# Kernel tuning notes

Hardware: AMD Instinct MI355X
Metric: run time of the kernel (lower is better)

## Reference

```python
import jax, jax.numpy as jnp
import numpy as np

L, B, S, E, H, V = 2, 64, 64, 1024, 1024, 32000


def _uni(key, shape, k):
    return jax.random.uniform(key, shape, jnp.float32, -k, k)


def setup_inputs() -> dict:
    key = jax.random.key(0)
    ks = jax.random.split(key, 16)
    k = 1.0 / np.sqrt(H)
    inp = {
        "inputs": jax.random.randint(ks[0], (S, B), 0, V),
        "hidden": jnp.zeros((L, B, H), jnp.float32),
        "emb": jax.random.uniform(ks[1], (V, E), jnp.float32, -0.1, 0.1),
        # per-layer GRU weights stacked on leading L axis (layer0 input = emb = H)
        "Wx": _uni(ks[2], (L, H, H), k),   # linear_W (no bias), used for r gate
        "Ur": _uni(ks[3], (L, H, H), k),
        "br": _uni(ks[4], (L, H), k),
        "Wz": _uni(ks[5], (L, H, H), k),
        "Uz": _uni(ks[6], (L, H, H), k),
        "bz": _uni(ks[7], (L, H), k),
        "Wh": _uni(ks[8], (L, H, H), k),
        "Uh": _uni(ks[9], (L, H, H), k),
        "bh": _uni(ks[10], (L, H), k),
        "dec_W": jax.random.uniform(ks[11], (V, H), jnp.float32, -0.1, 0.1),
        "dec_b": jnp.zeros((V,), jnp.float32),
    }
    return inp


def _gru_cell(x, h, Wx, Ur, br, Wz, Uz, bz, Wh, Uh, bh):
    # faithful to GRU_Hidden.forward (r gate uses linear_W, bias-free W projections)
    r = jax.nn.sigmoid(x @ Wx.T + h @ Ur.T + br)
    z = jax.nn.sigmoid(x @ Wz.T + h @ Uz.T + bz)
    h_cand = jnp.tanh(x @ Wh.T + (r * h) @ Uh.T + bh)
    return (1.0 - z) * h + z * h_cand


def reference(inputs, hidden, emb, Wx, Ur, br, Wz, Uz, bz, Wh, Uh, bh, dec_W, dec_b):
    x_embs = emb[inputs]  # [S, B, E]; dropout is identity (dp_keep_prob = 1.0)
    n_layers = Wx.shape[0]

    def step(h, x_t):
        new_h = []
        inp = x_t
        for l in range(n_layers):
            hl = _gru_cell(inp, h[l], Wx[l], Ur[l], br[l], Wz[l], Uz[l], bz[l], Wh[l], Uh[l], bh[l])
            new_h.append(hl)
            inp = hl
        logits_t = inp @ dec_W.T + dec_b  # [B, V]
        return jnp.stack(new_h), logits_t

    h_final, logits = jax.lax.scan(step, hidden, x_embs)
    return logits, h_final
```

## Files before the change

kernel.cpp:

```cpp
#include <hip/hip_runtime.h>

#define NB_REC 128
#define SBV    131072000

typedef __bf16 bf16x8 __attribute__((ext_vector_type(8)));
typedef float  f32x4  __attribute__((ext_vector_type(4)));
typedef unsigned short u16;

__device__ __forceinline__ u16 f2bf(float f) {
  union { float f; unsigned u; } c; c.f = f;
  return (u16)((c.u + 0x7fffu + ((c.u >> 16) & 1u)) >> 16);
}
__device__ __forceinline__ float sigm(float x) { return 1.f / (1.f + __expf(-x)); }
__device__ __forceinline__ float tanh_f(float x) { return 2.f / (1.f + __expf(-2.f * x)) - 1.f; }


__global__ void k_cvtv(const float* __restrict__ src, u16* __restrict__ dst, int n4) {
  const float4* s4 = (const float4*)src;
  ushort4* d4 = (ushort4*)dst;
  for (int i = blockIdx.x * blockDim.x + threadIdx.x; i < n4; i += gridDim.x * blockDim.x) {
    float4 v = s4[i];
    ushort4 o; o.x = f2bf(v.x); o.y = f2bf(v.y); o.z = f2bf(v.z); o.w = f2bf(v.w);
    d4[i] = o;
  }
}

__global__ void k_pack3(const float* __restrict__ sx, const float* __restrict__ sz,
                        const float* __restrict__ sh, int srcOff, u16* __restrict__ dst) {
  int i = blockIdx.x * blockDim.x + threadIdx.x;
  if (i >= 786432) return;
  int g = i >> 18;
  int r4 = i & 262143;
  const float* s = (g == 0 ? sx : (g == 1 ? sz : sh)) + srcOff;
  float4 v = ((const float4*)s)[r4];
  ushort4 o; o.x = f2bf(v.x); o.y = f2bf(v.y); o.z = f2bf(v.z); o.w = f2bf(v.w);
  ((ushort4*)dst)[i] = o;
}

__global__ void k_embed(const int* __restrict__ idx, const float* __restrict__ emb,
                        u16* __restrict__ xe) {
  int i = blockIdx.x * blockDim.x + threadIdx.x;
  if (i >= 1048576) return;
  int row = i >> 8, k4 = i & 255;
  int e = idx[row];
  float4 v = ((const float4*)emb)[(size_t)e * 256 + k4];
  ushort4 o; o.x = f2bf(v.x); o.y = f2bf(v.y); o.z = f2bf(v.z); o.w = f2bf(v.w);
  ((ushort4*)xe)[i] = o;
}

template<bool BIAS>
__global__ __launch_bounds__(256) void gemm_bt(const u16* __restrict__ A, const u16* __restrict__ Bm,
                                               float* __restrict__ C, const float* __restrict__ bias,
                                               int M, int N, int K, int mtiles) {
  __shared__ u16 As[128 * 32];
  __shared__ u16 Bs[128 * 32];
  const int tid = threadIdx.x;
  const int bm = blockIdx.x % mtiles, bn = blockIdx.x / mtiles;
  const int m0 = bm * 128, n0 = bn * 128;
  const int lane = tid & 63, w = tid >> 6, wm = w & 1, wn = w >> 1;
  const int la = lane & 15, lk = lane >> 4;
  const int srow = tid >> 2, sk = (tid & 3) * 8;
  f32x4 acc[4][4] = {};
  for (int kt = 0; kt < K; kt += 32) {
    const u16* srcA0 = A + (size_t)(m0 + srow) * K + kt + sk;
    const u16* srcA1 = A + (size_t)(m0 + srow + 64) * K + kt + sk;
    const u16* srcB0 = Bm + (size_t)(n0 + srow) * K + kt + sk;
    const u16* srcB1 = Bm + (size_t)(n0 + srow + 64) * K + kt + sk;
    __builtin_amdgcn_global_load_lds((const __attribute__((address_space(1))) void*)srcA0,
        (__attribute__((address_space(3))) void*)((char*)As + tid * 16), 16, 0, 0);
    __builtin_amdgcn_global_load_lds((const __attribute__((address_space(1))) void*)srcA1,
        (__attribute__((address_space(3))) void*)((char*)As + 4096 + tid * 16), 16, 0, 0);
    __builtin_amdgcn_global_load_lds((const __attribute__((address_space(1))) void*)srcB0,
        (__attribute__((address_space(3))) void*)((char*)Bs + tid * 16), 16, 0, 0);
    __builtin_amdgcn_global_load_lds((const __attribute__((address_space(1))) void*)srcB1,
        (__attribute__((address_space(3))) void*)((char*)Bs + 4096 + tid * 16), 16, 0, 0);
    __syncthreads();
    bf16x8 av[4], bv[4];
    #pragma unroll
    for (int m = 0; m < 4; ++m)
      av[m] = *(const bf16x8*)(As + (wm * 64 + m * 16 + la) * 32 + lk * 8);
    #pragma unroll
    for (int n = 0; n < 4; ++n)
      bv[n] = *(const bf16x8*)(Bs + (wn * 64 + n * 16 + la) * 32 + lk * 8);
    #pragma unroll
    for (int m = 0; m < 4; ++m)
      #pragma unroll
      for (int n = 0; n < 4; ++n)
        acc[m][n] = __builtin_amdgcn_mfma_f32_16x16x32_bf16(av[m], bv[n], acc[m][n], 0, 0, 0);
    __syncthreads();
  }
  #pragma unroll
  for (int n = 0; n < 4; ++n) {
    const int gc = n0 + wn * 64 + n * 16 + la;
    const float bb = BIAS ? bias[gc] : 0.f;
    #pragma unroll
    for (int m = 0; m < 4; ++m) {
      const int gr0 = m0 + wm * 64 + m * 16 + lk * 4;
      #pragma unroll
      for (int r = 0; r < 4; ++r)
        C[(size_t)(gr0 + r) * N + gc] = acc[m][n][r] + bb;
    }
  }
}


__device__ __forceinline__ void waitg64(const unsigned* f, unsigned tgt, int tid) {
  if (tgt && tid < 64) {
    unsigned g = 0;
    while (true) {
      bool ok = true;
      if (tid < 16) {
        uint4 v; const uint4* p = (const uint4*)f + tid;
        asm volatile("global_load_dwordx4 %0, %1, off sc1\ns_waitcnt vmcnt(0)"
                     : "=v"(v) : "v"(p) : "memory");
        ok = v.x >= tgt && v.y >= tgt && v.z >= tgt && v.w >= tgt;
      }
      if (__all(ok)) break;
      __builtin_amdgcn_s_sleep(1);
      if (++g > 1000000u) break;
    }
  }
  __syncthreads();
}

__device__ __forceinline__ void waitg2x(const unsigned* f0, unsigned t0,
                                        const unsigned* f1, unsigned t1, int tid) {
  if (tid < 64) {
    unsigned g = 0;
    while (true) {
      bool ok = true;
      if (tid < 32) {
        const unsigned* f = (tid < 16) ? f0 : f1;
        unsigned tgt = (tid < 16) ? t0 : t1;
        if (tgt) {
          uint4 v; const uint4* p = (const uint4*)f + (tid & 15);
          asm volatile("global_load_dwordx4 %0, %1, off sc1\ns_waitcnt vmcnt(0)"
                       : "=v"(v) : "v"(p) : "memory");
          ok = v.x >= tgt && v.y >= tgt && v.z >= tgt && v.w >= tgt;
        }
      }
      if (__all(ok)) break;
      __builtin_amdgcn_s_sleep(1);
      if (++g > 1000000u) break;
    }
  }
  __syncthreads();
}

__device__ __forceinline__ void arrive(unsigned* myFlag, unsigned val, int tid) {
  asm volatile("s_waitcnt vmcnt(0)" ::: "memory");
  __syncthreads();
  if (tid == 0)
    asm volatile("global_store_dword %0, %1, off sc1" :: "v"(myFlag), "v"(val) : "memory");
}

__global__ __launch_bounds__(256) void k_recur(
    const u16* __restrict__ hinitb,
    const float* __restrict__ hidden,
    const float* __restrict__ X0,
    const u16* __restrict__ Ucat0, const u16* __restrict__ Ucat1,
    const u16* __restrict__ Wcat1,
    const float* __restrict__ br, const float* __restrict__ bz, const float* __restrict__ bh,
    u16* __restrict__ H0seq, u16* __restrict__ H1seq,
    u16* __restrict__ RH0, u16* __restrict__ RH1,
    float* __restrict__ houtf,
    unsigned* flags) {
  extern __shared__ char sW[];
  const int tid = threadIdx.x, bid = blockIdx.x;
  const int layer = bid >> 6, jb = bid & 63, j0 = jb * 16;
  const int lane = tid & 63, w = tid >> 6;
  const int la = lane & 15, lk = lane >> 4;
  const int jl = j0 + la;
  const int row0 = w * 16;
  const u16* Ucat = layer ? Ucat1 : Ucat0;
  u16* Hseq = layer ? H1seq : H0seq;
  u16* RHl = layer ? RH1 : RH0;
  const u16* hinit = hinitb + layer * 65536;
  unsigned* fSelf = flags + layer * 64;
  const unsigned* fL0 = flags;
  unsigned* myFlag = fSelf + jb;

  __builtin_amdgcn_fence(__ATOMIC_ACQUIRE, "agent");

  const int xorv = (la & 7) << 4;
  for (int i = 0; i < 24; ++i) {
    int c = i * 256 + tid;
    int g = c >> 11, rem = c & 2047;
    int urow = rem >> 7, kc = rem & 127;
    uint4 v = *(const uint4*)(Ucat + ((size_t)((g << 10) + j0 + urow)) * 1024 + kc * 8);
    *(uint4*)(sW + (g << 15) + urow * 2048 + ((kc * 16) ^ ((urow & 7) << 4))) = v;
  }
  __syncthreads();
  const char* sWla = sW + la * 2048;

  float h_reg[4], z_reg[4];
  #pragma unroll
  for (int r = 0; r < 4; ++r)
    h_reg[r] = hidden[layer * 65536 + (row0 + lk * 4 + r) * 1024 + jl];
  const float bR = br[layer * 1024 + jl], bZ = bz[layer * 1024 + jl], bH = bh[layer * 1024 + jl];

  const u16* WrR = Wcat1 + (size_t)(j0 + la) * 1024 + lk * 8;
  const u16* WrZ = WrR + (size_t)1024 * 1024;
  const u16* WrH = WrR + (size_t)2048 * 1024;

  for (int t = 0; t < 64; ++t) {
    if (layer == 0) waitg64(fSelf, 2 * t, tid);
    else            waitg2x(fSelf, 2 * t, fL0, 2 * t + 2, tid);
    const u16* hsrc = (t == 0) ? hinit : (Hseq + (size_t)(t - 1) * 65536);
    const u16* ap = hsrc + (size_t)(row0 + la) * 1024 + lk * 8;
    f32x4 accR = {0.f, 0.f, 0.f, 0.f}, accZ = {0.f, 0.f, 0.f, 0.f};
    if (layer == 0) {
      #pragma unroll 8
      for (int ks = 0; ks < 32; ++ks) {
        const int kx = (ks * 64 + lk * 16) ^ xorv;
        bf16x8 a = *(const bf16x8*)(ap + ks * 32);
        accR = __builtin_amdgcn_mfma_f32_16x16x32_bf16(a, *(const bf16x8*)(sWla + kx), accR, 0, 0, 0);
        accZ = __builtin_amdgcn_mfma_f32_16x16x32_bf16(a, *(const bf16x8*)(sWla + 32768 + kx), accZ, 0, 0, 0);
      }
    } else {
      const u16* xp = H0seq + (size_t)t * 65536 + (size_t)(row0 + la) * 1024 + lk * 8;
      #pragma unroll 4
      for (int ks = 0; ks < 32; ++ks) {
        const int kx = (ks * 64 + lk * 16) ^ xorv;
        bf16x8 a = *(const bf16x8*)(ap + ks * 32);
        bf16x8 x = *(const bf16x8*)(xp + ks * 32);
        accR = __builtin_amdgcn_mfma_f32_16x16x32_bf16(a, *(const bf16x8*)(sWla + kx), accR, 0, 0, 0);
        accZ = __builtin_amdgcn_mfma_f32_16x16x32_bf16(a, *(const bf16x8*)(sWla + 32768 + kx), accZ, 0, 0, 0);
        accR = __builtin_amdgcn_mfma_f32_16x16x32_bf16(x, *(const bf16x8*)(WrR + ks * 32), accR, 0, 0, 0);
        accZ = __builtin_amdgcn_mfma_f32_16x16x32_bf16(x, *(const bf16x8*)(WrZ + ks * 32), accZ, 0, 0, 0);
      }
    }
    #pragma unroll
    for (int r = 0; r < 4; ++r) {
      const int row = row0 + lk * 4 + r;
      float pr = accR[r] + bR, pz = accZ[r] + bZ;
      if (layer == 0) {
        const float* xf = X0 + (size_t)(t * 64 + row) * 3072 + jl;
        pr += xf[0]; pz += xf[1024];
      }
      float rv = sigm(pr);
      z_reg[r] = sigm(pz);
      unsigned v = f2bf(rv * h_reg[r]);
      u16* p = RHl + (size_t)(t * 64 + row) * 1024 + jl;
      asm volatile("global_store_short %0, %1, off sc1" :: "v"(p), "v"(v));
    }
    arrive(myFlag, 2 * t + 1, tid);
    waitg64(fSelf, 2 * t + 1, tid);
    const u16* rp = RHl + (size_t)t * 65536 + (size_t)(row0 + la) * 1024 + lk * 8;
    f32x4 accH = {0.f, 0.f, 0.f, 0.f};
    if (layer == 0) {
      #pragma unroll 8
      for (int ks = 0; ks < 32; ++ks) {
        const int kx = (ks * 64 + lk * 16) ^ xorv;
        bf16x8 a = *(const bf16x8*)(rp + ks * 32);
        accH = __builtin_amdgcn_mfma_f32_16x16x32_bf16(a, *(const bf16x8*)(sWla + 65536 + kx), accH, 0, 0, 0);
      }
    } else {
      const u16* xp = H0seq + (size_t)t * 65536 + (size_t)(row0 + la) * 1024 + lk * 8;
      #pragma unroll 8
      for (int ks = 0; ks < 32; ++ks) {
        const int kx = (ks * 64 + lk * 16) ^ xorv;
        bf16x8 a = *(const bf16x8*)(rp + ks * 32);
        bf16x8 x = *(const bf16x8*)(xp + ks * 32);
        accH = __builtin_amdgcn_mfma_f32_16x16x32_bf16(a, *(const bf16x8*)(sWla + 65536 + kx), accH, 0, 0, 0);
        accH = __builtin_amdgcn_mfma_f32_16x16x32_bf16(x, *(const bf16x8*)(WrH + ks * 32), accH, 0, 0, 0);
      }
    }
    #pragma unroll
    for (int r = 0; r < 4; ++r) {
      const int row = row0 + lk * 4 + r;
      float pre = accH[r] + bH;
      if (layer == 0) pre += X0[(size_t)(t * 64 + row) * 3072 + 2048 + jl];
      float hc = tanh_f(pre);
      float hn = h_reg[r] + z_reg[r] * (hc - h_reg[r]);
      h_reg[r] = hn;
      unsigned v = f2bf(hn);
      u16* p = Hseq + (size_t)(t * 64 + row) * 1024 + jl;
      asm volatile("global_store_short %0, %1, off sc1" :: "v"(p), "v"(v));
      if (t == 63) houtf[layer * 65536 + row * 1024 + jl] = hn;
    }
    arrive(myFlag, 2 * t + 2, tid);
  }
}

extern "C" void kernel_launch(void* const* d_in, const int* in_sizes, int n_in,
                              void* d_out, int out_size, void* d_ws, size_t ws_size,
                              hipStream_t stream) {
  const int* inputs = (const int*)d_in[0];
  const float* hidden = (const float*)d_in[1];
  const float* emb = (const float*)d_in[2];
  const float* Wx = (const float*)d_in[3];
  const float* Ur = (const float*)d_in[4];
  const float* br = (const float*)d_in[5];
  const float* Wz = (const float*)d_in[6];
  const float* Uz = (const float*)d_in[7];
  const float* bz = (const float*)d_in[8];
  const float* Wh = (const float*)d_in[9];
  const float* Uh = (const float*)d_in[10];
  const float* bh = (const float*)d_in[11];
  const float* decW = (const float*)d_in[12];
  const float* decb = (const float*)d_in[13];
  float* out = (float*)d_out;

  char* ws = (char*)d_ws;
  size_t off = 0;
  auto alloc = [&](size_t bytes) { char* p = ws + off; off += (bytes + 255) & ~(size_t)255; return p; };
  unsigned* flags = (unsigned*)alloc(4096);
  u16* hinitb = (u16*)alloc((size_t)2 * 64 * 1024 * 2);
  u16* xe     = (u16*)alloc((size_t)4096 * 1024 * 2);
  u16* Wcat0b = (u16*)alloc((size_t)3072 * 1024 * 2);
  u16* Wcat1b = (u16*)alloc((size_t)3072 * 1024 * 2);
  u16* Ucat0b = (u16*)alloc((size_t)3072 * 1024 * 2);
  u16* Ucat1b = (u16*)alloc((size_t)3072 * 1024 * 2);
  u16* decWb  = (u16*)alloc((size_t)32000 * 1024 * 2);
  float* X0   = (float*)alloc((size_t)4096 * 3072 * 4);
  u16* H0seq  = (u16*)alloc((size_t)4096 * 1024 * 2);
  u16* H1seq  = (u16*)alloc((size_t)4096 * 1024 * 2);
  u16* RH0    = (u16*)alloc((size_t)4096 * 1024 * 2);
  u16* RH1    = (u16*)alloc((size_t)4096 * 1024 * 2);

  hipMemsetAsync(flags, 0, 4096, stream);
  k_cvtv<<<128, 256, 0, stream>>>(hidden, hinitb, 32768);
  k_pack3<<<3072, 256, 0, stream>>>(Wx, Wz, Wh, 0, Wcat0b);
  k_pack3<<<3072, 256, 0, stream>>>(Wx, Wz, Wh, 1048576, Wcat1b);
  k_pack3<<<3072, 256, 0, stream>>>(Ur, Uz, Uh, 0, Ucat0b);
  k_pack3<<<3072, 256, 0, stream>>>(Ur, Uz, Uh, 1048576, Ucat1b);
  k_embed<<<4096, 256, 0, stream>>>(inputs, emb, xe);
  k_cvtv<<<4096, 256, 0, stream>>>(decW, decWb, 8192000);

  gemm_bt<false><<<768, 256, 0, stream>>>(xe, Wcat0b, X0, nullptr, 4096, 3072, 1024, 32);

  (void)hipFuncSetAttribute(reinterpret_cast<const void*>(&k_recur),
                            hipFuncAttributeMaxDynamicSharedMemorySize, 98304);
  k_recur<<<NB_REC, 256, 98304, stream>>>(hinitb, hidden, X0, Ucat0b, Ucat1b, Wcat1b,
                                          br, bz, bh, H0seq, H1seq, RH0, RH1,
                                          out + (size_t)SBV, flags);

  gemm_bt<true><<<8000, 256, 0, stream>>>(H1seq, decWb, out, decb, 4096, 32000, 1024, 32);
}
```

Baseline: 2.888 ms.

## Fuse decoder GEMM into recurrent kernel, overlapping per-timestep with recurrence

The separate decoder GEMM launch is removed. 125 extra blocks are added to the persistent recurrent kernel, and each one computes logits for its 256 vocab columns. Each extra block waits on the layer-1 flags for step t, then runs the 64x256 tile for that timestep, so decoding overlaps the serial recurrence. The unroll factors in the recurrence loops are also raised. The risk is that the decoder blocks lose LDS reuse (operands are read straight from global) and compete for memory bandwidth and CUs with the latency-critical recurrence; 253 blocks must also be co-resident for the spin-wait scheme to work.

```diff
diff --git a/kernel.cpp b/kernel.cpp
--- a/kernel.cpp
+++ b/kernel.cpp
@@ -1,7 +1,6 @@
 #include <hip/hip_runtime.h>
 
-#define NB_REC 128
-#define SBV    131072000
+#define SBV 131072000
 
 typedef __bf16 bf16x8 __attribute__((ext_vector_type(8)));
 typedef float  f32x4  __attribute__((ext_vector_type(4)));
@@ -48,10 +47,8 @@
   ((ushort4*)xe)[i] = o;
 }
 
-template<bool BIAS>
 __global__ __launch_bounds__(256) void gemm_bt(const u16* __restrict__ A, const u16* __restrict__ Bm,
-                                               float* __restrict__ C, const float* __restrict__ bias,
-                                               int M, int N, int K, int mtiles) {
+                                               float* __restrict__ C, int M, int N, int K, int mtiles) {
   __shared__ u16 As[128 * 32];
   __shared__ u16 Bs[128 * 32];
   const int tid = threadIdx.x;
@@ -92,13 +89,12 @@
   #pragma unroll
   for (int n = 0; n < 4; ++n) {
     const int gc = n0 + wn * 64 + n * 16 + la;
-    const float bb = BIAS ? bias[gc] : 0.f;
     #pragma unroll
     for (int m = 0; m < 4; ++m) {
       const int gr0 = m0 + wm * 64 + m * 16 + lk * 4;
       #pragma unroll
       for (int r = 0; r < 4; ++r)
-        C[(size_t)(gr0 + r) * N + gc] = acc[m][n][r] + bb;
+        C[(size_t)(gr0 + r) * N + gc] = acc[m][n][r];
     }
   }
 }
@@ -154,7 +150,7 @@
     asm volatile("global_store_dword %0, %1, off sc1" :: "v"(myFlag), "v"(val) : "memory");
 }
 
-__global__ __launch_bounds__(256) void k_recur(
+__global__ __launch_bounds__(256) void k_fused(
     const u16* __restrict__ hinitb,
     const float* __restrict__ hidden,
     const float* __restrict__ X0,
@@ -163,13 +159,61 @@
     const float* __restrict__ br, const float* __restrict__ bz, const float* __restrict__ bh,
     u16* __restrict__ H0seq, u16* __restrict__ H1seq,
     u16* __restrict__ RH0, u16* __restrict__ RH1,
-    float* __restrict__ houtf,
+    const u16* __restrict__ decWb,
+    const float* __restrict__ decb,
+    float* __restrict__ out,
     unsigned* flags) {
   extern __shared__ char sW[];
   const int tid = threadIdx.x, bid = blockIdx.x;
-  const int layer = bid >> 6, jb = bid & 63, j0 = jb * 16;
   const int lane = tid & 63, w = tid >> 6;
   const int la = lane & 15, lk = lane >> 4;
+
+  __builtin_amdgcn_fence(__ATOMIC_ACQUIRE, "agent");
+
+  if (bid >= 128) {
+    const int d = bid - 128;
+    const int c0 = d * 256 + w * 64;
+    float bb[4];
+    #pragma unroll
+    for (int nf = 0; nf < 4; ++nf) bb[nf] = decb[c0 + nf * 16 + la];
+    const u16* Bp[4];
+    #pragma unroll
+    for (int nf = 0; nf < 4; ++nf)
+      Bp[nf] = decWb + (size_t)(c0 + nf * 16 + la) * 1024 + lk * 8;
+    for (int t = 0; t < 64; ++t) {
+      waitg64(flags + 64, 2 * t + 2, tid);
+      const u16* Ab = H1seq + (size_t)t * 65536;
+      const u16* Ap[4];
+      #pragma unroll
+      for (int mf = 0; mf < 4; ++mf) Ap[mf] = Ab + (mf * 16 + la) * 1024 + lk * 8;
+      f32x4 acc[4][4] = {};
+      #pragma unroll 4
+      for (int ks = 0; ks < 32; ++ks) {
+        bf16x8 av[4], bv[4];
+        #pragma unroll
+        for (int mf = 0; mf < 4; ++mf) av[mf] = *(const bf16x8*)(Ap[mf] + ks * 32);
+        #pragma unroll
+        for (int nf = 0; nf < 4; ++nf) bv[nf] = *(const bf16x8*)(Bp[nf] + ks * 32);
+        #pragma unroll
+        for (int mf = 0; mf < 4; ++mf)
+          #pragma unroll
+          for (int nf = 0; nf < 4; ++nf)
+            acc[mf][nf] = __builtin_amdgcn_mfma_f32_16x16x32_bf16(av[mf], bv[nf], acc[mf][nf], 0, 0, 0);
+      }
+      #pragma unroll
+      for (int mf = 0; mf < 4; ++mf)
+        #pragma unroll
+        for (int nf = 0; nf < 4; ++nf) {
+          const size_t rb = (size_t)(t * 64 + mf * 16 + lk * 4) * 32000 + c0 + nf * 16 + la;
+          #pragma unroll
+          for (int r = 0; r < 4; ++r)
+            out[rb + (size_t)r * 32000] = acc[mf][nf][r] + bb[nf];
+        }
+    }
+    return;
+  }
+
+  const int layer = bid >> 6, jb = bid & 63, j0 = jb * 16;
   const int jl = j0 + la;
   const int row0 = w * 16;
   const u16* Ucat = layer ? Ucat1 : Ucat0;
@@ -179,8 +223,7 @@
   unsigned* fSelf = flags + layer * 64;
   const unsigned* fL0 = flags;
   unsigned* myFlag = fSelf + jb;
-
-  __builtin_amdgcn_fence(__ATOMIC_ACQUIRE, "agent");
+  float* houtf = out + (size_t)SBV;
 
   const int xorv = (la & 7) << 4;
   for (int i = 0; i < 24; ++i) {
@@ -210,7 +253,7 @@
     const u16* ap = hsrc + (size_t)(row0 + la) * 1024 + lk * 8;
     f32x4 accR = {0.f, 0.f, 0.f, 0.f}, accZ = {0.f, 0.f, 0.f, 0.f};
     if (layer == 0) {
-      #pragma unroll 8
+      #pragma unroll 16
       for (int ks = 0; ks < 32; ++ks) {
         const int kx = (ks * 64 + lk * 16) ^ xorv;
         bf16x8 a = *(const bf16x8*)(ap + ks * 32);
@@ -219,7 +262,7 @@
       }
     } else {
       const u16* xp = H0seq + (size_t)t * 65536 + (size_t)(row0 + la) * 1024 + lk * 8;
-      #pragma unroll 4
+      #pragma unroll 8
       for (int ks = 0; ks < 32; ++ks) {
         const int kx = (ks * 64 + lk * 16) ^ xorv;
         bf16x8 a = *(const bf16x8*)(ap + ks * 32);
@@ -249,7 +292,7 @@
     const u16* rp = RHl + (size_t)t * 65536 + (size_t)(row0 + la) * 1024 + lk * 8;
     f32x4 accH = {0.f, 0.f, 0.f, 0.f};
     if (layer == 0) {
-      #pragma unroll 8
+      #pragma unroll 16
       for (int ks = 0; ks < 32; ++ks) {
         const int kx = (ks * 64 + lk * 16) ^ xorv;
         bf16x8 a = *(const bf16x8*)(rp + ks * 32);
@@ -328,13 +371,11 @@
   k_embed<<<4096, 256, 0, stream>>>(inputs, emb, xe);
   k_cvtv<<<4096, 256, 0, stream>>>(decW, decWb, 8192000);
 
-  gemm_bt<false><<<768, 256, 0, stream>>>(xe, Wcat0b, X0, nullptr, 4096, 3072, 1024, 32);
-
-  (void)hipFuncSetAttribute(reinterpret_cast<const void*>(&k_recur),
+  gemm_bt<<<768, 256, 0, stream>>>(xe, Wcat0b, X0, 4096, 3072, 1024, 32);
+
+  (void)hipFuncSetAttribute(reinterpret_cast<const void*>(&k_fused),
                             hipFuncAttributeMaxDynamicSharedMemorySize, 98304);
-  k_recur<<<NB_REC, 256, 98304, stream>>>(hinitb, hidden, X0, Ucat0b, Ucat1b, Wcat1b,
-                                          br, bz, bh, H0seq, H1seq, RH0, RH1,
-                                          out + (size_t)SBV, flags);
-
-  gemm_bt<true><<<8000, 256, 0, stream>>>(H1seq, decWb, out, decb, 4096, 32000, 1024, 32);
-}
+  k_fused<<<253, 256, 98304, stream>>>(hinitb, hidden, X0, Ucat0b, Ucat1b, Wcat1b,
+                                       br, bz, bh, H0seq, H1seq, RH0, RH1,
+                                       decWb, decb, out, flags);
+}
```

Measured after the change: 2.480 ms. -14.2%, faster.
